# Optimization experiments

Measured on AMD Instinct MI355X. Metric: run time of the kernel, lower is better.

Reference implementation:

```python
import jax, jax.numpy as jnp
import numpy as np

N = 50000
E = 500000
R = 8
IN_DIM = 128
HID = 128
NUM_CLASSES = 16
NUM_GRAPHS = 64


def setup_inputs() -> dict:
    key = jax.random.key(0)
    ks = jax.random.split(key, 12)
    x = jax.random.normal(ks[0], (N, IN_DIM), dtype=jnp.float32)
    edge_index = jax.random.randint(ks[1], (2, E), 0, N)
    edge_type = jax.random.randint(ks[2], (E,), 0, R)
    batch = jnp.sort(jax.random.randint(ks[3], (N,), 0, NUM_GRAPHS))
    s = 1.0 / np.sqrt(IN_DIM)
    W1 = jax.random.uniform(ks[4], (R, IN_DIM, HID), minval=-s, maxval=s, dtype=jnp.float32)
    root1 = jax.random.uniform(ks[5], (IN_DIM, HID), minval=-s, maxval=s, dtype=jnp.float32)
    b1 = jnp.zeros((HID,), jnp.float32)
    s2 = 1.0 / np.sqrt(HID)
    W2 = jax.random.uniform(ks[6], (R, HID, HID), minval=-s2, maxval=s2, dtype=jnp.float32)
    root2 = jax.random.uniform(ks[7], (HID, HID), minval=-s2, maxval=s2, dtype=jnp.float32)
    b2 = jnp.zeros((HID,), jnp.float32)
    linW = jax.random.uniform(ks[8], (HID, NUM_CLASSES), minval=-s2, maxval=s2, dtype=jnp.float32)
    linb = jnp.zeros((NUM_CLASSES,), jnp.float32)
    return {"x": x, "edge_index": edge_index, "edge_type": edge_type, "batch": batch,
            "W1": W1, "root1": root1, "b1": b1, "W2": W2, "root2": root2, "b2": b2,
            "linW": linW, "linb": linb}


def rgcn_conv(x, src, dst, rel, W, root, b):
    # Per-relation transform of ALL nodes once: [R, N, H] (avoids per-edge weight gather)
    xW = jnp.einsum('nd,rdh->rnh', x, W)
    msg = xW[rel, src]                      # [E, H] gather per edge
    # PyG RGCNConv default aggr='mean': mean over neighbors per (dst, relation)
    seg = dst * R + rel                     # composite segment id
    cnt = jax.ops.segment_sum(jnp.ones((msg.shape[0],), msg.dtype), seg, num_segments=N * R)
    norm = 1.0 / jnp.maximum(cnt, 1.0)
    msg = msg * norm[seg][:, None]
    agg = jax.ops.segment_sum(msg, dst, num_segments=N)  # sum over relations folds in
    return agg + x @ root + b


def global_mean_pool(x, batch):
    sums = jax.ops.segment_sum(x, batch, num_segments=NUM_GRAPHS)
    cnt = jax.ops.segment_sum(jnp.ones((x.shape[0],), x.dtype), batch, num_segments=NUM_GRAPHS)
    return sums / jnp.maximum(cnt, 1.0)[:, None]


def reference(x, edge_index, edge_type, batch, W1, root1, b1, W2, root2, b2, linW, linb):
    src, dst = edge_index[0], edge_index[1]
    h = jax.nn.relu(rgcn_conv(x, src, dst, edge_type, W1, root1, b1))
    h = jax.nn.relu(rgcn_conv(h, src, dst, edge_type, W2, root2, b2))
    pooled = global_mean_pool(h, batch)     # [G, HID]
    return pooled @ linW + linb             # [G, NUM_CLASSES]
```

## Files before the change

kernel.cpp:

```cpp
#include <hip/hip_runtime.h>
#include <hip/hip_bf16.h>
#include <stdint.h>

#define N_NODES 50000
#define N_EDGES 500000
#define R_REL 8
#define HID 128
#define KIN 128
#define KOUT 1152
#define N8 400000
#define NPAD 50048
#define NUM_GRAPHS 64
#define NUM_CLASSES 16

typedef __attribute__((ext_vector_type(8))) short bf16x8;
typedef __attribute__((ext_vector_type(4))) float f32x4;

__device__ __forceinline__ uint16_t f2bf(float f) {
  uint32_t u = __float_as_uint(f);
  u += 0x7FFFu + ((u >> 16) & 1u);
  return (uint16_t)(u >> 16);
}
__device__ __forceinline__ float bf2f(uint32_t b) {
  return __uint_as_float(b << 16);
}
__device__ __forceinline__ uint32_t pack2bf(float a, float b) {
  return (uint32_t)f2bf(a) | ((uint32_t)f2bf(b) << 16);
}

#define HIST_B 1954
#define BND_B 196
#define PW_B 576
__global__ __launch_bounds__(256) void k_prep(const int* __restrict__ ei, const int* __restrict__ et,
                                              int* __restrict__ deg8,
                                              const int* __restrict__ batch,
                                              int* __restrict__ gs, int* __restrict__ ge,
                                              const float* __restrict__ W1, const float* __restrict__ root1,
                                              uint16_t* __restrict__ Wf1,
                                              const float* __restrict__ W2, const float* __restrict__ root2,
                                              uint16_t* __restrict__ Wf2) {
  int b = blockIdx.x;
  if (b < HIST_B) {
    int i = b * 256 + threadIdx.x;
    if (i < N_EDGES) atomicAdd(&deg8[ei[N_EDGES + i] * R_REL + et[i]], 1);
    return;
  }
  b -= HIST_B;
  if (b < BND_B) {
    int i = b * 256 + threadIdx.x;
    if (i < N_NODES) {
      int g = batch[i];
      if (i == 0) gs[g] = 0;
      else { int pg = batch[i - 1]; if (pg != g) { ge[pg] = i; gs[g] = i; } }
      if (i == N_NODES - 1) ge[g] = N_NODES;
    }
    return;
  }
  b -= BND_B;
  {
    const float* W    = (b < PW_B) ? W1 : W2;
    const float* root = (b < PW_B) ? root1 : root2;
    uint16_t*    Wf   = (b < PW_B) ? Wf1 : Wf2;
    int idx = (b % PW_B) * 256 + threadIdx.x;
    int e = idx & 7, L = (idx >> 3) & 63, f = idx >> 9;
    int quad = L >> 4, l16 = L & 15;
    int kc = f & 3, nt = (f >> 2) & 7, s = f >> 5;
    int k = kc * 32 + quad * 8 + e;
    int no = nt * 16 + l16;
    float v = (s < R_REL) ? W[((size_t)s * KIN + k) * HID + no] : root[(size_t)k * HID + no];
    Wf[idx] = f2bf(v);
  }
}

__global__ __launch_bounds__(256) void k_scan1(const int* __restrict__ deg8, int* __restrict__ offs8,
                                               int* __restrict__ bsum) {
  __shared__ int sh[256];
  int t = threadIdx.x;
  int base = blockIdx.x * 1024 + t * 4;
  int v[4]; int s = 0;
  #pragma unroll
  for (int i = 0; i < 4; ++i) { int idx = base + i; v[i] = (idx < N8) ? deg8[idx] : 0; s += v[i]; }
  sh[t] = s;
  __syncthreads();
  for (int d = 1; d < 256; d <<= 1) {
    int add = (t >= d) ? sh[t - d] : 0;
    __syncthreads();
    sh[t] += add;
    __syncthreads();
  }
  int run = sh[t] - s;
  if (t == 255) bsum[blockIdx.x] = sh[255];
  #pragma unroll
  for (int i = 0; i < 4; ++i) { int idx = base + i; if (idx < N8) offs8[idx] = run; run += v[i]; }
}

__global__ __launch_bounds__(512) void k_scan2(int* __restrict__ bsum, int nb) {
  __shared__ int sh[512];
  int t = threadIdx.x;
  int v = (t < nb) ? bsum[t] : 0;
  sh[t] = v;
  __syncthreads();
  for (int d = 1; d < 512; d <<= 1) {
    int add = (t >= d) ? sh[t - d] : 0;
    __syncthreads();
    sh[t] += add;
    __syncthreads();
  }
  if (t < nb) bsum[t] = sh[t] - v;
}

__global__ __launch_bounds__(256) void k_scan3(int* __restrict__ offs8, int* __restrict__ nxt,
                                               const int* __restrict__ bsum) {
  int i = blockIdx.x * 256 + threadIdx.x;
  if (i < N8) {
    int o = offs8[i] + bsum[i >> 10];
    offs8[i] = o;
    nxt[i] = o;
  }
  if (i == 0) offs8[N8] = N_EDGES;
}

__global__ __launch_bounds__(256) void k_scatter(const int* __restrict__ ei, const int* __restrict__ et,
                                                 const int* __restrict__ deg8, int* __restrict__ nxt,
                                                 uint32_t* __restrict__ epack, float* __restrict__ wgt) {
  int i = blockIdx.x * 256 + threadIdx.x;
  if (i < N_EDGES) {
    int rel = et[i];
    int key = ei[N_EDGES + i] * R_REL + rel;
    int p = atomicAdd(&nxt[key], 1);
    epack[p] = (uint32_t)ei[i] | ((uint32_t)rel << 16);
    wgt[p] = 1.0f / (float)deg8[key];
  }
}

template<bool IN_BF16>
__global__ __launch_bounds__(64) void k_gemmY(const void* __restrict__ in,
                                              const uint16_t* __restrict__ Wf,
                                              uint16_t* __restrict__ Y) {
  int L = threadIdx.x;
  int quad = L >> 4, l16 = L & 15;
  int blockM = blockIdx.x * 64;

  bf16x8 af[4][4];
  #pragma unroll
  for (int i = 0; i < 4; ++i) {
    int row = blockM + i * 16 + l16;
    bool valid = row < N_NODES;
    #pragma unroll
    for (int kc = 0; kc < 4; ++kc) {
      if (IN_BF16) {
        uint4 v = {0u, 0u, 0u, 0u};
        if (valid) v = *(const uint4*)((const uint16_t*)in + (size_t)row * KIN + kc * 32 + quad * 8);
        union { uint4 u; bf16x8 b; } cv; cv.u = v;
        af[i][kc] = cv.b;
      } else {
        float4 a = {0.f,0.f,0.f,0.f}, c = {0.f,0.f,0.f,0.f};
        if (valid) {
          const float* p = (const float*)in + (size_t)row * KIN + kc * 32 + quad * 8;
          a = *(const float4*)p;
          c = *(const float4*)(p + 4);
        }
        bf16x8 r;
        r[0] = (short)f2bf(a.x); r[1] = (short)f2bf(a.y); r[2] = (short)f2bf(a.z); r[3] = (short)f2bf(a.w);
        r[4] = (short)f2bf(c.x); r[5] = (short)f2bf(c.y); r[6] = (short)f2bf(c.z); r[7] = (short)f2bf(c.w);
        af[i][kc] = r;
      }
    }
  }

  #pragma unroll 1
  for (int s = 0; s < 9; ++s) {
    f32x4 acc[4][8];
    #pragma unroll
    for (int i = 0; i < 4; ++i)
      #pragma unroll
      for (int nt = 0; nt < 8; ++nt) acc[i][nt] = (f32x4){0.f, 0.f, 0.f, 0.f};
    #pragma unroll
    for (int kc = 0; kc < 4; ++kc) {
      bf16x8 bfr[8];
      #pragma unroll
      for (int nt = 0; nt < 8; ++nt) {
        int f = (s * 8 + nt) * 4 + kc;
        bfr[nt] = *(const bf16x8*)(Wf + (size_t)f * 512 + L * 8);
      }
      #pragma unroll
      for (int i = 0; i < 4; ++i)
        #pragma unroll
        for (int nt = 0; nt < 8; ++nt)
          acc[i][nt] = __builtin_amdgcn_mfma_f32_16x16x32_bf16(af[i][kc], bfr[nt], acc[i][nt], 0, 0, 0);
    }
    #pragma unroll
    for (int i = 0; i < 4; ++i) {
      #pragma unroll
      for (int nt = 0; nt < 8; ++nt) {
        int col = s * 128 + nt * 16 + l16;
        #pragma unroll
        for (int rg = 0; rg < 4; ++rg) {
          int row = blockM + i * 16 + quad * 4 + rg;
          Y[(size_t)row * KOUT + col] = f2bf(acc[i][nt][rg]);
        }
      }
    }
  }
}

template<bool OUT_BF16>
__global__ __launch_bounds__(256) void k_msg(const uint16_t* __restrict__ Y,
                                             const uint32_t* __restrict__ epack,
                                             const float* __restrict__ wgt,
                                             const int* __restrict__ offs8,
                                             const float* __restrict__ bias,
                                             void* __restrict__ hout) {
  int n = (blockIdx.x * 256 + threadIdx.x) >> 6;
  n = __builtin_amdgcn_readfirstlane(n);
  int L = threadIdx.x & 63;
  if (n >= N_NODES) return;
  uint32_t rv = *(const uint32_t*)(Y + (size_t)n * KOUT + R_REL * HID + L * 2);
  float ax = bf2f(rv & 0xFFFFu), ay = bf2f(rv >> 16);
  int o0 = offs8[n * R_REL];
  int o8 = offs8[n * R_REL + R_REL];
  for (int g = o0; g < o8; g += 8) {
    int m8 = min(8, o8 - g);
    uint32_t pv[8]; float wv[8]; uint32_t vv[8];
    #pragma unroll
    for (int i = 0; i < 8; ++i) if (i < m8) { pv[i] = epack[g + i]; wv[i] = wgt[g + i]; }
    #pragma unroll
    for (int i = 0; i < 8; ++i) if (i < m8)
      vv[i] = *(const uint32_t*)(Y + (size_t)(pv[i] & 0xFFFFu) * KOUT + (pv[i] >> 16) * HID + L * 2);
    #pragma unroll
    for (int i = 0; i < 8; ++i) if (i < m8) {
      ax += bf2f(vv[i] & 0xFFFFu) * wv[i];
      ay += bf2f(vv[i] >> 16) * wv[i];
    }
  }
  float2 bb = *(const float2*)(bias + L * 2);
  ax = fmaxf(ax + bb.x, 0.f);
  ay = fmaxf(ay + bb.y, 0.f);
  if (OUT_BF16)
    *(uint32_t*)((uint16_t*)hout + (size_t)n * HID + L * 2) = pack2bf(ax, ay);
  else {
    float2 o2 = {ax, ay};
    *(float2*)((float*)hout + (size_t)n * HID + L * 2) = o2;
  }
}

__global__ __launch_bounds__(256) void k_poolpart(const float* __restrict__ h,
                                                  const int* __restrict__ gs, const int* __restrict__ ge,
                                                  float* __restrict__ psum) {
  __shared__ float red[HID];
  int g = blockIdx.x >> 2, p = blockIdx.x & 3;
  int c = threadIdx.x & 127, ph = threadIdx.x >> 7;
  int s = gs[g], e = ge[g];
  int len = e - s;
  int quarter = (len + 3) >> 2;
  int n0 = s + p * quarter;
  int n1 = min(n0 + quarter, e);
  float acc = 0.f;
  for (int n = n0 + ph; n < n1; n += 2) acc += h[(size_t)n * HID + c];
  if (ph == 1) red[c] = acc;
  __syncthreads();
  if (ph == 0 && n0 < n1) atomicAdd(&psum[g * HID + c], acc + red[c]);
}

__global__ __launch_bounds__(1024) void k_final(const float* __restrict__ psum,
                                                const int* __restrict__ gs, const int* __restrict__ ge,
                                                const float* __restrict__ linW, const float* __restrict__ linb,
                                                float* __restrict__ out) {
  int i = threadIdx.x;
  int g = i >> 4, c = i & 15;
  float inv = 1.f / fmaxf((float)(ge[g] - gs[g]), 1.f);
  float s = 0.f;
  #pragma unroll 8
  for (int k = 0; k < HID; ++k) s += psum[g * HID + k] * linW[k * NUM_CLASSES + c];
  out[i] = s * inv + linb[c];
}

extern "C" void kernel_launch(void* const* d_in, const int* in_sizes, int n_in,
                              void* d_out, int out_size, void* d_ws, size_t ws_size,
                              hipStream_t stream) {
  const float* x     = (const float*)d_in[0];
  const int*   ei    = (const int*)d_in[1];
  const int*   et    = (const int*)d_in[2];
  const int*   batch = (const int*)d_in[3];
  const float* W1    = (const float*)d_in[4];
  const float* root1 = (const float*)d_in[5];
  const float* b1    = (const float*)d_in[6];
  const float* W2    = (const float*)d_in[7];
  const float* root2 = (const float*)d_in[8];
  const float* b2    = (const float*)d_in[9];
  const float* linW  = (const float*)d_in[10];
  const float* linb  = (const float*)d_in[11];
  float* out = (float*)d_out;

  char* ws = (char*)d_ws;
  size_t off = 0;
  auto alloc = [&](size_t bytes) -> char* {
    char* p = ws + off;
    off += (bytes + 255) & ~(size_t)255;
    return p;
  };
  int*      deg8  = (int*)alloc((size_t)N8 * 4);
  int*      gb    = (int*)alloc(2 * NUM_GRAPHS * 4);
  float*    psum  = (float*)alloc((size_t)NUM_GRAPHS * HID * 4);
  size_t zbytes = (size_t)N8 * 4 + 512 + (size_t)NUM_GRAPHS * HID * 4;
  int*      gs    = gb;
  int*      ge    = gb + NUM_GRAPHS;
  int*      offs8 = (int*)alloc((size_t)(N8 + 1) * 4);
  int*      nxt   = (int*)alloc((size_t)N8 * 4);
  int*      bsum  = (int*)alloc(512 * 4);
  uint32_t* epack = (uint32_t*)alloc((size_t)N_EDGES * 4);
  float*    wgt   = (float*)alloc((size_t)N_EDGES * 4);
  uint16_t* Wf1   = (uint16_t*)alloc((size_t)KOUT * KIN * 2);
  uint16_t* Wf2   = (uint16_t*)alloc((size_t)KOUT * KIN * 2);
  uint16_t* Y     = (uint16_t*)alloc((size_t)NPAD * KOUT * 2);
  uint16_t* h1b   = (uint16_t*)alloc((size_t)N_NODES * HID * 2);
  float*    h2    = (float*)alloc((size_t)N_NODES * HID * 4);

  hipMemsetAsync(deg8, 0, zbytes, stream);

  int nb = (N8 + 1023) / 1024;
  k_prep<<<HIST_B + BND_B + 2 * PW_B, 256, 0, stream>>>(
      ei, et, deg8, batch, gs, ge, W1, root1, Wf1, W2, root2, Wf2);
  k_scan1<<<nb, 256, 0, stream>>>(deg8, offs8, bsum);
  k_scan2<<<1, 512, 0, stream>>>(bsum, nb);
  k_scan3<<<(N8 + 255) / 256, 256, 0, stream>>>(offs8, nxt, bsum);
  k_scatter<<<(N_EDGES + 255) / 256, 256, 0, stream>>>(ei, et, deg8, nxt, epack, wgt);

  k_gemmY<false><<<NPAD / 64, 64, 0, stream>>>(x, Wf1, Y);
  k_msg<true ><<<N_NODES / 4, 256, 0, stream>>>(Y, epack, wgt, offs8, b1, h1b);
  k_gemmY<true ><<<NPAD / 64, 64, 0, stream>>>(h1b, Wf2, Y);
  k_msg<false><<<N_NODES / 4, 256, 0, stream>>>(Y, epack, wgt, offs8, b2, h2);

  k_poolpart<<<4 * NUM_GRAPHS, 256, 0, stream>>>(h2, gs, ge, psum);
  k_final<<<1, 1024, 0, stream>>>(psum, gs, ge, linW, linb, out);
}
```

Measured before the change: 317.5 us.

## Aggregate-then-transform: fuse per-relation neighbor mean with GEMM in one kernel

Reorders each RGCN layer from transforming all nodes by every relation weight and then gathering per edge, to first gathering raw bf16 features into per-relation aggregates in shared memory and then running one K=1152 GEMM per node tile. This removes the large N×1152 intermediate Y and its write and read traffic, and gathers 128-wide rows instead of slices of a wide matrix. The input x is converted to bf16 inside the prep kernel. In exchange the per-relation aggregates are rounded to bf16 before the GEMM, and the GEMM is small-tiled (32 nodes per block) with weights re-read from global memory by every block.

```diff
diff --git a/kernel.cpp b/kernel.cpp
--- a/kernel.cpp
+++ b/kernel.cpp
@@ -9,9 +9,13 @@
 #define KIN 128
 #define KOUT 1152
 #define N8 400000
-#define NPAD 50048
 #define NUM_GRAPHS 64
 #define NUM_CLASSES 16
+
+#define BN 32
+#define LDA 1160
+#define NKC 36
+#define NBLK 1563
 
 typedef __attribute__((ext_vector_type(8))) short bf16x8;
 typedef __attribute__((ext_vector_type(4))) float f32x4;
@@ -31,6 +35,7 @@
 #define HIST_B 1954
 #define BND_B 196
 #define PW_B 576
+#define CVT_B 3125
 __global__ __launch_bounds__(256) void k_prep(const int* __restrict__ ei, const int* __restrict__ et,
                                               int* __restrict__ deg8,
                                               const int* __restrict__ batch,
@@ -38,7 +43,8 @@
                                               const float* __restrict__ W1, const float* __restrict__ root1,
                                               uint16_t* __restrict__ Wf1,
                                               const float* __restrict__ W2, const float* __restrict__ root2,
-                                              uint16_t* __restrict__ Wf2) {
+                                              uint16_t* __restrict__ Wf2,
+                                              const float* __restrict__ x, uint16_t* __restrict__ xb) {
   int b = blockIdx.x;
   if (b < HIST_B) {
     int i = b * 256 + threadIdx.x;
@@ -57,18 +63,30 @@
     return;
   }
   b -= BND_B;
-  {
+  if (b < 2 * PW_B) {
     const float* W    = (b < PW_B) ? W1 : W2;
     const float* root = (b < PW_B) ? root1 : root2;
     uint16_t*    Wf   = (b < PW_B) ? Wf1 : Wf2;
     int idx = (b % PW_B) * 256 + threadIdx.x;
     int e = idx & 7, L = (idx >> 3) & 63, f = idx >> 9;
     int quad = L >> 4, l16 = L & 15;
-    int kc = f & 3, nt = (f >> 2) & 7, s = f >> 5;
-    int k = kc * 32 + quad * 8 + e;
-    int no = nt * 16 + l16;
-    float v = (s < R_REL) ? W[((size_t)s * KIN + k) * HID + no] : root[(size_t)k * HID + no];
+    int nt = f & 7, kc = f >> 3;
+    int kk = kc * 32 + quad * 8 + e;
+    int s = kk >> 7, k = kk & 127;
+    int col = nt * 16 + l16;
+    float v = (s < R_REL) ? W[((size_t)s * KIN + k) * HID + col] : root[(size_t)k * HID + col];
     Wf[idx] = f2bf(v);
+    return;
+  }
+  b -= 2 * PW_B;
+  {
+    int i = b * 256 + threadIdx.x;
+    const float4* p = (const float4*)x + (size_t)i * 2;
+    float4 a = p[0], c = p[1];
+    uint4 o;
+    o.x = pack2bf(a.x, a.y); o.y = pack2bf(a.z, a.w);
+    o.z = pack2bf(c.x, c.y); o.w = pack2bf(c.z, c.w);
+    *(uint4*)(xb + (size_t)i * 8) = o;
   }
 }
 
@@ -133,114 +151,115 @@
   }
 }
 
-template<bool IN_BF16>
-__global__ __launch_bounds__(64) void k_gemmY(const void* __restrict__ in,
-                                              const uint16_t* __restrict__ Wf,
-                                              uint16_t* __restrict__ Y) {
-  int L = threadIdx.x;
+template<bool OUT_BF16>
+__global__ __launch_bounds__(256, 2) void k_fused(const uint16_t* __restrict__ hin,
+                                                  const uint32_t* __restrict__ epack,
+                                                  const float* __restrict__ wgt,
+                                                  const int* __restrict__ offs8,
+                                                  const uint16_t* __restrict__ Wf,
+                                                  const float* __restrict__ bias,
+                                                  void* __restrict__ hout) {
+  __shared__ __align__(16) uint16_t As[BN * LDA];
+  int t = threadIdx.x;
+  int w = __builtin_amdgcn_readfirstlane(t >> 6);
+  int L = t & 63;
   int quad = L >> 4, l16 = L & 15;
-  int blockM = blockIdx.x * 64;
-
-  bf16x8 af[4][4];
-  #pragma unroll
-  for (int i = 0; i < 4; ++i) {
-    int row = blockM + i * 16 + l16;
-    bool valid = row < N_NODES;
+  int node0 = blockIdx.x * BN;
+
+  {
+    bf16x8 z = 0;
     #pragma unroll
-    for (int kc = 0; kc < 4; ++kc) {
-      if (IN_BF16) {
-        uint4 v = {0u, 0u, 0u, 0u};
-        if (valid) v = *(const uint4*)((const uint16_t*)in + (size_t)row * KIN + kc * 32 + quad * 8);
-        union { uint4 u; bf16x8 b; } cv; cv.u = v;
-        af[i][kc] = cv.b;
-      } else {
-        float4 a = {0.f,0.f,0.f,0.f}, c = {0.f,0.f,0.f,0.f};
-        if (valid) {
-          const float* p = (const float*)in + (size_t)row * KIN + kc * 32 + quad * 8;
-          a = *(const float4*)p;
-          c = *(const float4*)(p + 4);
+    for (int i = 0; i < 18; ++i) ((bf16x8*)As)[i * 256 + t] = z;
+    if (t < 32) ((bf16x8*)As)[18 * 256 + t] = z;
+  }
+  __syncthreads();
+
+  #pragma unroll 1
+  for (int ni = 0; ni < 8; ++ni) {
+    int nl = w * 8 + ni;
+    int n = node0 + nl;
+    if (n >= N_NODES) break;
+    uint16_t* Arow = As + nl * LDA;
+    *(uint32_t*)(Arow + R_REL * HID + L * 2) =
+        *(const uint32_t*)(hin + (size_t)n * HID + L * 2);
+    int o0 = offs8[n * R_REL];
+    int o8 = offs8[n * R_REL + R_REL];
+    float ax = 0.f, ay = 0.f;
+    int cur = -1;
+    for (int g = o0; g < o8; g += 8) {
+      int m8 = min(8, o8 - g);
+      uint32_t pv[8]; float wv[8]; uint32_t vv[8];
+      #pragma unroll
+      for (int i = 0; i < 8; ++i) if (i < m8) { pv[i] = epack[g + i]; wv[i] = wgt[g + i]; }
+      #pragma unroll
+      for (int i = 0; i < 8; ++i) if (i < m8)
+        vv[i] = *(const uint32_t*)(hin + (size_t)(pv[i] & 0xFFFFu) * HID + L * 2);
+      #pragma unroll
+      for (int i = 0; i < 8; ++i) if (i < m8) {
+        int r = (int)(pv[i] >> 16);
+        if (r != cur) {
+          if (cur >= 0) *(uint32_t*)(Arow + cur * HID + L * 2) = pack2bf(ax, ay);
+          ax = 0.f; ay = 0.f; cur = r;
         }
-        bf16x8 r;
-        r[0] = (short)f2bf(a.x); r[1] = (short)f2bf(a.y); r[2] = (short)f2bf(a.z); r[3] = (short)f2bf(a.w);
-        r[4] = (short)f2bf(c.x); r[5] = (short)f2bf(c.y); r[6] = (short)f2bf(c.z); r[7] = (short)f2bf(c.w);
-        af[i][kc] = r;
+        ax += bf2f(vv[i] & 0xFFFFu) * wv[i];
+        ay += bf2f(vv[i] >> 16) * wv[i];
       }
     }
-  }
+    if (cur >= 0) *(uint32_t*)(Arow + cur * HID + L * 2) = pack2bf(ax, ay);
+  }
+  __syncthreads();
+
+  f32x4 acc[2][2];
+  #pragma unroll
+  for (int m = 0; m < 2; ++m)
+    #pragma unroll
+    for (int j = 0; j < 2; ++j) acc[m][j] = (f32x4){0.f, 0.f, 0.f, 0.f};
+
+  const uint16_t* wp = Wf + (size_t)(w * 2) * 512 + (size_t)L * 8;
+  const uint16_t* ap = As + l16 * LDA + quad * 8;
+
+  bf16x8 b0 = *(const bf16x8*)wp;
+  bf16x8 b1 = *(const bf16x8*)(wp + 512);
+  bf16x8 a0 = *(const bf16x8*)ap;
+  bf16x8 a1 = *(const bf16x8*)(ap + 16 * LDA);
 
   #pragma unroll 1
-  for (int s = 0; s < 9; ++s) {
-    f32x4 acc[4][8];
+  for (int kc = 0; kc < NKC - 1; ++kc) {
+    const uint16_t* wpn = wp + (size_t)(kc + 1) * 4096;
+    bf16x8 nb0 = *(const bf16x8*)wpn;
+    bf16x8 nb1 = *(const bf16x8*)(wpn + 512);
+    const uint16_t* apn = ap + (kc + 1) * 32;
+    bf16x8 na0 = *(const bf16x8*)apn;
+    bf16x8 na1 = *(const bf16x8*)(apn + 16 * LDA);
+    acc[0][0] = __builtin_amdgcn_mfma_f32_16x16x32_bf16(a0, b0, acc[0][0], 0, 0, 0);
+    acc[1][0] = __builtin_amdgcn_mfma_f32_16x16x32_bf16(a1, b0, acc[1][0], 0, 0, 0);
+    acc[0][1] = __builtin_amdgcn_mfma_f32_16x16x32_bf16(a0, b1, acc[0][1], 0, 0, 0);
+    acc[1][1] = __builtin_amdgcn_mfma_f32_16x16x32_bf16(a1, b1, acc[1][1], 0, 0, 0);
+    a0 = na0; a1 = na1; b0 = nb0; b1 = nb1;
+  }
+  acc[0][0] = __builtin_amdgcn_mfma_f32_16x16x32_bf16(a0, b0, acc[0][0], 0, 0, 0);
+  acc[1][0] = __builtin_amdgcn_mfma_f32_16x16x32_bf16(a1, b0, acc[1][0], 0, 0, 0);
+  acc[0][1] = __builtin_amdgcn_mfma_f32_16x16x32_bf16(a0, b1, acc[0][1], 0, 0, 0);
+  acc[1][1] = __builtin_amdgcn_mfma_f32_16x16x32_bf16(a1, b1, acc[1][1], 0, 0, 0);
+
+  #pragma unroll
+  for (int m = 0; m < 2; ++m) {
     #pragma unroll
-    for (int i = 0; i < 4; ++i)
+    for (int j = 0; j < 2; ++j) {
+      int col = w * 32 + j * 16 + l16;
+      float bv = bias[col];
       #pragma unroll
-      for (int nt = 0; nt < 8; ++nt) acc[i][nt] = (f32x4){0.f, 0.f, 0.f, 0.f};
-    #pragma unroll
-    for (int kc = 0; kc < 4; ++kc) {
-      bf16x8 bfr[8];
-      #pragma unroll
-      for (int nt = 0; nt < 8; ++nt) {
-        int f = (s * 8 + nt) * 4 + kc;
-        bfr[nt] = *(const bf16x8*)(Wf + (size_t)f * 512 + L * 8);
-      }
-      #pragma unroll
-      for (int i = 0; i < 4; ++i)
-        #pragma unroll
-        for (int nt = 0; nt < 8; ++nt)
-          acc[i][nt] = __builtin_amdgcn_mfma_f32_16x16x32_bf16(af[i][kc], bfr[nt], acc[i][nt], 0, 0, 0);
-    }
-    #pragma unroll
-    for (int i = 0; i < 4; ++i) {
-      #pragma unroll
-      for (int nt = 0; nt < 8; ++nt) {
-        int col = s * 128 + nt * 16 + l16;
-        #pragma unroll
-        for (int rg = 0; rg < 4; ++rg) {
-          int row = blockM + i * 16 + quad * 4 + rg;
-          Y[(size_t)row * KOUT + col] = f2bf(acc[i][nt][rg]);
+      for (int rg = 0; rg < 4; ++rg) {
+        int row = node0 + m * 16 + quad * 4 + rg;
+        if (row < N_NODES) {
+          float v = fmaxf(acc[m][j][rg] + bv, 0.f);
+          if (OUT_BF16)
+            ((uint16_t*)hout)[(size_t)row * HID + col] = f2bf(v);
+          else
+            ((float*)hout)[(size_t)row * HID + col] = v;
         }
       }
     }
-  }
-}
-
-template<bool OUT_BF16>
-__global__ __launch_bounds__(256) void k_msg(const uint16_t* __restrict__ Y,
-                                             const uint32_t* __restrict__ epack,
-                                             const float* __restrict__ wgt,
-                                             const int* __restrict__ offs8,
-                                             const float* __restrict__ bias,
-                                             void* __restrict__ hout) {
-  int n = (blockIdx.x * 256 + threadIdx.x) >> 6;
-  n = __builtin_amdgcn_readfirstlane(n);
-  int L = threadIdx.x & 63;
-  if (n >= N_NODES) return;
-  uint32_t rv = *(const uint32_t*)(Y + (size_t)n * KOUT + R_REL * HID + L * 2);
-  float ax = bf2f(rv & 0xFFFFu), ay = bf2f(rv >> 16);
-  int o0 = offs8[n * R_REL];
-  int o8 = offs8[n * R_REL + R_REL];
-  for (int g = o0; g < o8; g += 8) {
-    int m8 = min(8, o8 - g);
-    uint32_t pv[8]; float wv[8]; uint32_t vv[8];
-    #pragma unroll
-    for (int i = 0; i < 8; ++i) if (i < m8) { pv[i] = epack[g + i]; wv[i] = wgt[g + i]; }
-    #pragma unroll
-    for (int i = 0; i < 8; ++i) if (i < m8)
-      vv[i] = *(const uint32_t*)(Y + (size_t)(pv[i] & 0xFFFFu) * KOUT + (pv[i] >> 16) * HID + L * 2);
-    #pragma unroll
-    for (int i = 0; i < 8; ++i) if (i < m8) {
-      ax += bf2f(vv[i] & 0xFFFFu) * wv[i];
-      ay += bf2f(vv[i] >> 16) * wv[i];
-    }
-  }
-  float2 bb = *(const float2*)(bias + L * 2);
-  ax = fmaxf(ax + bb.x, 0.f);
-  ay = fmaxf(ay + bb.y, 0.f);
-  if (OUT_BF16)
-    *(uint32_t*)((uint16_t*)hout + (size_t)n * HID + L * 2) = pack2bf(ax, ay);
-  else {
-    float2 o2 = {ax, ay};
-    *(float2*)((float*)hout + (size_t)n * HID + L * 2) = o2;
   }
 }
 
@@ -312,24 +331,22 @@
   float*    wgt   = (float*)alloc((size_t)N_EDGES * 4);
   uint16_t* Wf1   = (uint16_t*)alloc((size_t)KOUT * KIN * 2);
   uint16_t* Wf2   = (uint16_t*)alloc((size_t)KOUT * KIN * 2);
-  uint16_t* Y     = (uint16_t*)alloc((size_t)NPAD * KOUT * 2);
+  uint16_t* xb    = (uint16_t*)alloc((size_t)N_NODES * HID * 2);
   uint16_t* h1b   = (uint16_t*)alloc((size_t)N_NODES * HID * 2);
   float*    h2    = (float*)alloc((size_t)N_NODES * HID * 4);
 
   hipMemsetAsync(deg8, 0, zbytes, stream);
 
   int nb = (N8 + 1023) / 1024;
-  k_prep<<<HIST_B + BND_B + 2 * PW_B, 256, 0, stream>>>(
-      ei, et, deg8, batch, gs, ge, W1, root1, Wf1, W2, root2, Wf2);
+  k_prep<<<HIST_B + BND_B + 2 * PW_B + CVT_B, 256, 0, stream>>>(
+      ei, et, deg8, batch, gs, ge, W1, root1, Wf1, W2, root2, Wf2, x, xb);
   k_scan1<<<nb, 256, 0, stream>>>(deg8, offs8, bsum);
   k_scan2<<<1, 512, 0, stream>>>(bsum, nb);
   k_scan3<<<(N8 + 255) / 256, 256, 0, stream>>>(offs8, nxt, bsum);
   k_scatter<<<(N_EDGES + 255) / 256, 256, 0, stream>>>(ei, et, deg8, nxt, epack, wgt);
 
-  k_gemmY<false><<<NPAD / 64, 64, 0, stream>>>(x, Wf1, Y);
-  k_msg<true ><<<N_NODES / 4, 256, 0, stream>>>(Y, epack, wgt, offs8, b1, h1b);
-  k_gemmY<true ><<<NPAD / 64, 64, 0, stream>>>(h1b, Wf2, Y);
-  k_msg<false><<<N_NODES / 4, 256, 0, stream>>>(Y, epack, wgt, offs8, b2, h2);
+  k_fused<true ><<<NBLK, 256, 0, stream>>>(xb,  epack, wgt, offs8, Wf1, b1, h1b);
+  k_fused<false><<<NBLK, 256, 0, stream>>>(h1b, epack, wgt, offs8, Wf2, b2, h2);
 
   k_poolpart<<<4 * NUM_GRAPHS, 256, 0, stream>>>(h2, gs, ge, psum);
   k_final<<<1, 1024, 0, stream>>>(psum, gs, ge, linW, linb, out);
```

New measurement: 409.3 us. 1.29x slower.
